# Performance work log

Measured on AMD Instinct MI355X. Metric: run time of the kernel, lower is better.

Reference implementation:

```python
import jax, jax.numpy as jnp
import numpy as np

N = 20000      # nodes (human PPI network scale)
E = 640000     # edges (avg degree 32)
PE, GOS, PROT = 128, 128, 480
OM_DIMS = [3, 3, 24, 24]          # transcriptome, proteome, effectome, interactome
D = 384                           # latent_space_dimension = 128 * 3 (jk 'cat')
H = 128                           # hidden_channels per layer
NEG_SLOPE = 0.1


def setup_inputs() -> dict:
    key = jax.random.key(0)
    ks = jax.random.split(key, 64)
    rn = lambda k, shp, s=0.05: jax.random.normal(k, shp, jnp.float32) * s
    inp = {
        "x": jax.random.normal(ks[0], (N, PE + GOS + PROT), jnp.float32),
        "x_ft": jax.random.normal(ks[1], (N, sum(OM_DIMS)), jnp.float32),
        "edge_index": jax.random.randint(ks[2], (2, E), 0, N),
    }
    i = 3
    def lin(fin, fout, name):
        nonlocal i
        inp["W_" + name] = rn(ks[i], (fin, fout)); inp["b_" + name] = jnp.zeros((fout,), jnp.float32)
        i += 1
    lin(PE, D, "pe"); lin(GOS, D, "gos"); lin(PROT, D, "prot")
    for j, d in enumerate(OM_DIMS):
        lin(d, D, f"om{j}")
    dims = [D, H, H, H]
    for j in range(3):
        lin(dims[j], dims[j + 1], f"c{j}")   # feature-branch GCN convs
        lin(dims[j], dims[j + 1], f"o{j}")   # omics-branch GCN convs
    lin(2 * D, D, "lat")
    lin(D, H, "drug"); lin(D, H, "dis")
    lin(H, 2, "odrug"); lin(H, 2, "odis")
    return inp


def _gcn(x, W, b, src, dst, deg_inv):
    # GCNConv(improved=True): A_hat = A + 2I, sym norm D^-1/2 A_hat D^-1/2
    h = x @ W                                  # [N, F_out]
    coef = deg_inv[src] * deg_inv[dst]         # [E]
    agg = jax.ops.segment_sum(h[src] * coef[:, None], dst, num_segments=N)
    agg = agg + h * (2.0 * deg_inv * deg_inv)[:, None]   # self loops (weight 2)
    return agg + b


def reference(x, x_ft, edge_index,
              W_pe, b_pe, W_gos, b_gos, W_prot, b_prot,
              W_om0, b_om0, W_om1, b_om1, W_om2, b_om2, W_om3, b_om3,
              W_c0, b_c0, W_o0, b_o0, W_c1, b_c1, W_o1, b_o1, W_c2, b_c2, W_o2, b_o2,
              W_lat, b_lat, W_drug, b_drug, W_dis, b_dis,
              W_odrug, b_odrug, W_odis, b_odis):
    act = lambda t: jax.nn.leaky_relu(t, NEG_SLOPE)
    src, dst = edge_index[0], edge_index[1]
    deg = jax.ops.segment_sum(jnp.ones((E,), jnp.float32), dst, num_segments=N) + 2.0
    deg_inv = jax.lax.rsqrt(deg)

    # encoders (features branch): pe | gosemsim | prot_emb slices of x
    pe = x[:, :PE]; gos = x[:, PE:PE + GOS]; prot = x[:, PE + GOS:PE + GOS + PROT]
    h = act(pe @ W_pe + b_pe + gos @ W_gos + b_gos + prot @ W_prot + b_prot)

    # encoders (omics branch): 3|3|24|24 slices of x_ft
    offs = np.cumsum([0] + OM_DIMS)
    Wom = [W_om0, W_om1, W_om2, W_om3]; bom = [b_om0, b_om1, b_om2, b_om3]
    g = act(sum(x_ft[:, offs[j]:offs[j + 1]] @ Wom[j] + bom[j] for j in range(4)))

    Wc = [W_c0, W_c1, W_c2]; bc = [b_c0, b_c1, b_c2]
    Wo = [W_o0, W_o1, W_o2]; bo = [b_o0, b_o1, b_o2]
    hs, gs = [], []
    for j in range(3):
        h = act(_gcn(h, Wc[j], bc[j], src, dst, deg_inv)); hs.append(h)
        g = act(_gcn(g, Wo[j], bo[j], src, dst, deg_inv)); gs.append(g)
    jk = jnp.concatenate(hs, axis=-1)          # [N, 384]
    jk_om = jnp.concatenate(gs, axis=-1)       # [N, 384]

    z = act(jnp.concatenate([jk, jk_om], axis=-1) @ W_lat + b_lat)  # [N, 384]
    drug = act(z @ W_drug + b_drug) @ W_odrug + b_odrug             # [N, 2]
    dis = act(z @ W_dis + b_dis) @ W_odis + b_odis                  # [N, 2]
    return jnp.concatenate([drug, dis], axis=-1)                    # [N, 4]
```

## Files before the change

kernel.cpp:

```cpp
#include <hip/hip_runtime.h>
#include <cstdint>

#define NN 20000
#define NNP 20096
#define NE 640000
#define NEG_SLOPE 0.1f
#define NSCAN 79
#define NSL 8
#define NPSL 2500
#define FBPS 160
#define NPART 8

typedef unsigned short ushort_t;
typedef __attribute__((ext_vector_type(8))) short short8;
typedef __attribute__((ext_vector_type(4))) float f32x4;

__device__ __forceinline__ unsigned short f2bf(float f) {
    union { float f; unsigned u; } v; v.f = f;
    unsigned r = v.u + 0x7fffu + ((v.u >> 16) & 1u);
    return (unsigned short)(r >> 16);
}
__device__ __forceinline__ float bflo(unsigned u) { return __uint_as_float(u << 16); }
__device__ __forceinline__ float bfhi(unsigned u) { return __uint_as_float(u & 0xffff0000u); }

__device__ __forceinline__ int swz(int r) { return (r ^ (r >> 2)) & 3; }

__device__ __forceinline__ void gld_lds16(const void* g, void* l) {
    __builtin_amdgcn_global_load_lds(
        (const __attribute__((address_space(1))) void*)g,
        (__attribute__((address_space(3))) void*)l,
        16, 0, 0);
}

#define O_CAT   0
#define O_OM    282624
#define O_C0    307200
#define O_O0    356352
#define O_C1    405504
#define O_O1    421888
#define O_C2    438272
#define O_O2    454656
#define O_LAT   471040
#define O_HEADS 765952
#define WT_TOTAL 864256

#define PACK_TOTAL (WT_TOTAL + 384 + 384 + 256)
#define CVT_T1 (NN * 736 / 4)
#define P1_CNTB (NSL * FBPS)
#define P1_CVTB ((CVT_T1 + NN * 64 + 255) / 256)
#define P1_PKB  (PACK_TOTAL / 256)

__global__ __launch_bounds__(256) void phase1(
    const int* __restrict__ esrc, const int* __restrict__ edst, int* __restrict__ cnt8,
    const float* __restrict__ x, const float* __restrict__ xft,
    ushort_t* __restrict__ xb, ushort_t* __restrict__ xftb,
    const float* __restrict__ Wpe, const float* __restrict__ Wgos, const float* __restrict__ Wprot,
    const float* __restrict__ bpe, const float* __restrict__ bgos, const float* __restrict__ bprot,
    const float* __restrict__ Wom0, const float* __restrict__ Wom1,
    const float* __restrict__ Wom2, const float* __restrict__ Wom3,
    const float* __restrict__ bom0, const float* __restrict__ bom1,
    const float* __restrict__ bom2, const float* __restrict__ bom3,
    const float* __restrict__ Wc0, const float* __restrict__ Wo0,
    const float* __restrict__ Wc1, const float* __restrict__ Wo1,
    const float* __restrict__ Wc2, const float* __restrict__ Wo2,
    const float* __restrict__ Wlat,
    const float* __restrict__ Wdrug, const float* __restrict__ Wdis,
    const float* __restrict__ bdrug, const float* __restrict__ bdis,
    ushort_t* __restrict__ Wt, float* __restrict__ bcat, float* __restrict__ bomc,
    float* __restrict__ bheads)
{
    int bx = blockIdx.x;
    if (bx < P1_CNTB) {
        const int slice = bx & (NSL - 1);
        const int blk = bx >> 3;
        const int lo = slice * NPSL, hi = lo + NPSL;
        for (int e = blk * 256 + threadIdx.x; e < NE; e += FBPS * 256) {
            int d = edst[e];
            if (d >= lo && d < hi) {
                int p = (unsigned)esrc[e] / 2500u;
                atomicAdd(&cnt8[d * NPART + p], 1);
            }
        }
        return;
    }
    bx -= P1_CNTB;
    if (bx < P1_CVTB) {
        int i = bx * 256 + threadIdx.x;
        if (i < CVT_T1) {
            int base = i * 4;
            float4 v = *reinterpret_cast<const float4*>(&x[base]);
            unsigned long long p = (unsigned long long)f2bf(v.x)
                                 | ((unsigned long long)f2bf(v.y) << 16)
                                 | ((unsigned long long)f2bf(v.z) << 32)
                                 | ((unsigned long long)f2bf(v.w) << 48);
            *reinterpret_cast<unsigned long long*>(&xb[base]) = p;
            return;
        }
        i -= CVT_T1;
        if (i < NN * 64) {
            int r = i >> 6, c = i & 63;
            float v = (c < 54) ? xft[r * 54 + c] : 0.f;
            xftb[i] = f2bf(v);
        }
        return;
    }
    bx -= P1_CVTB;
    {
        int i = bx * 256 + threadIdx.x;
        if (i < 282624) {
            int m = i / 736, k = i % 736;
            float v = (k < 128) ? Wpe[k * 384 + m]
                    : (k < 256) ? Wgos[(k - 128) * 384 + m]
                                : Wprot[(k - 256) * 384 + m];
            Wt[O_CAT + i] = f2bf(v);
            return;
        }
        i -= 282624;
        if (i < 24576) {
            int m = i / 64, k = i % 64;
            float v = (k < 3)  ? Wom0[k * 384 + m]
                    : (k < 6)  ? Wom1[(k - 3) * 384 + m]
                    : (k < 30) ? Wom2[(k - 6) * 384 + m]
                    : (k < 54) ? Wom3[(k - 30) * 384 + m] : 0.f;
            Wt[O_OM + i] = f2bf(v);
            return;
        }
        i -= 24576;
        if (i < 49152) { int m = i / 384, k = i % 384; Wt[O_C0 + i] = f2bf(Wc0[k * 128 + m]); return; }
        i -= 49152;
        if (i < 49152) { int m = i / 384, k = i % 384; Wt[O_O0 + i] = f2bf(Wo0[k * 128 + m]); return; }
        i -= 49152;
        if (i < 16384) { int m = i / 128, k = i % 128; Wt[O_C1 + i] = f2bf(Wc1[k * 128 + m]); return; }
        i -= 16384;
        if (i < 16384) { int m = i / 128, k = i % 128; Wt[O_O1 + i] = f2bf(Wo1[k * 128 + m]); return; }
        i -= 16384;
        if (i < 16384) { int m = i / 128, k = i % 128; Wt[O_C2 + i] = f2bf(Wc2[k * 128 + m]); return; }
        i -= 16384;
        if (i < 16384) { int m = i / 128, k = i % 128; Wt[O_O2 + i] = f2bf(Wo2[k * 128 + m]); return; }
        i -= 16384;
        if (i < 294912) { int m = i / 768, k = i % 768; Wt[O_LAT + i] = f2bf(Wlat[k * 384 + m]); return; }
        i -= 294912;
        if (i < 98304) {
            int m = i / 384, k = i % 384;
            float v = (m < 128) ? Wdrug[k * 128 + m] : Wdis[k * 128 + (m - 128)];
            Wt[O_HEADS + i] = f2bf(v);
            return;
        }
        i -= 98304;
        if (i < 384) { bcat[i] = bpe[i] + bgos[i] + bprot[i]; return; }
        i -= 384;
        if (i < 384) { bomc[i] = bom0[i] + bom1[i] + bom2[i] + bom3[i]; return; }
        i -= 384;
        if (i < 256) { bheads[i] = (i < 128) ? bdrug[i] : bdis[i - 128]; return; }
    }
}

__global__ __launch_bounds__(256) void scan_blocksums(const int* __restrict__ cnt8, int* __restrict__ bsum,
                                                      float* __restrict__ deg_inv)
{
    __shared__ int s[256];
    int t = threadIdx.x, i = blockIdx.x * 256 + t;
    int v = 0;
    if (i < NN) {
        uint4 a = *reinterpret_cast<const uint4*>(&cnt8[i * NPART]);
        uint4 b = *reinterpret_cast<const uint4*>(&cnt8[i * NPART + 4]);
        v = (int)(a.x + a.y + a.z + a.w + b.x + b.y + b.z + b.w);
        deg_inv[i] = rsqrtf((float)v + 2.0f);
    }
    s[t] = v;
    __syncthreads();
    for (int off = 128; off; off >>= 1) {
        if (t < off) s[t] += s[t + off];
        __syncthreads();
    }
    if (t == 0) bsum[blockIdx.x] = s[0];
}

__global__ __launch_bounds__(256) void scan_apply(const int* __restrict__ cnt8, const int* __restrict__ bsum,
                                                  int* __restrict__ ofsN, int* __restrict__ cursor8)
{
    __shared__ int s[256];
    __shared__ int sb[NSCAN];
    int t = threadIdx.x, i = blockIdx.x * 256 + t;
    if (t < NSCAN) sb[t] = bsum[t];
    __syncthreads();
    if (t == 0) {
        int run = 0;
        for (int b = 0; b < NSCAN; b++) { int x2 = sb[b]; sb[b] = run; run += x2; }
        if (blockIdx.x == 0) ofsN[NN] = run;
    }
    __syncthreads();
    const int boff = sb[blockIdx.x];

    int c[NPART];
    int v = 0;
    if (i < NN) {
        uint4 a = *reinterpret_cast<const uint4*>(&cnt8[i * NPART]);
        uint4 b = *reinterpret_cast<const uint4*>(&cnt8[i * NPART + 4]);
        c[0] = a.x; c[1] = a.y; c[2] = a.z; c[3] = a.w;
        c[4] = b.x; c[5] = b.y; c[6] = b.z; c[7] = b.w;
#pragma unroll
        for (int p = 0; p < NPART; p++) v += c[p];
    }
    s[t] = v;
    __syncthreads();
    for (int off = 1; off < 256; off <<= 1) {
        int u = (t >= off) ? s[t - off] : 0;
        __syncthreads();
        s[t] += u;
        __syncthreads();
    }
    if (i < NN) {
        int run = s[t] - v + boff;
        ofsN[i] = run;
#pragma unroll
        for (int p = 0; p < NPART; p++) { cursor8[i * NPART + p] = run; run += c[p]; }
    }
}

__global__ __launch_bounds__(256) void fill_csr_sliced(
    const int* __restrict__ src, const int* __restrict__ dst,
    const float* __restrict__ deg_inv, int* __restrict__ cursor8,
    uint2* __restrict__ csr_pk)
{
    const int slice = blockIdx.x & (NSL - 1);
    const int blk = blockIdx.x >> 3;
    const int lo = slice * NPSL, hi = lo + NPSL;
    for (int e = blk * 256 + threadIdx.x; e < NE; e += FBPS * 256) {
        int d = dst[e];
        if (d >= lo && d < hi) {
            int s = src[e];
            int pp = (unsigned)s / 2500u;
            int p = atomicAdd(&cursor8[d * NPART + pp], 1);
            float cf = deg_inv[s] * deg_inv[d];
            csr_pk[p] = make_uint2((unsigned)s * 512u, __float_as_uint(cf));
        }
    }
}

template<int BN>
__device__ __forceinline__ void gemm_core(
    ushort_t* As, ushort_t* Bs,
    const ushort_t* __restrict__ A, int lda,
    const ushort_t* __restrict__ Wt, int K, int row0, int col0,
    f32x4 (&acc)[4][(BN == 128) ? 4 : 2])
{
    constexpr int BK = 32;
    constexpr int NI = (BN == 128) ? 4 : 2;

    const int t = threadIdx.x;
    const int w = t >> 6, lane = t & 63;
    const int wr = w >> 1, wc = w & 1;
    const int m16 = lane & 15, quad = lane >> 4;
    const int sr = lane >> 2;
    const int pgrp = lane & 3;

#pragma unroll
    for (int mi = 0; mi < 4; mi++)
#pragma unroll
        for (int ni = 0; ni < NI; ni++) acc[mi][ni] = (f32x4)0.f;

    for (int k0 = 0; k0 < K; k0 += BK) {
#pragma unroll
        for (int p = 0; p < 2; p++) {
            int c = p * 4 + w;
            int r = c * 16 + sr;
            int q = pgrp ^ swz(r);
            gld_lds16(&A[(size_t)(row0 + r) * lda + k0 + q * 8], &As[c * 512]);
        }
#pragma unroll
        for (int p = 0; p < BN / 64; p++) {
            int c = p * 4 + w;
            int r = c * 16 + sr;
            int q = pgrp ^ swz(r);
            gld_lds16(&Wt[(size_t)(col0 + r) * K + k0 + q * 8], &Bs[c * 512]);
        }
        __syncthreads();

        short8 af[4], bfr[NI];
#pragma unroll
        for (int mi = 0; mi < 4; mi++) {
            int r = wr * 64 + mi * 16 + m16;
            int p = quad ^ swz(r);
            af[mi] = *reinterpret_cast<const short8*>(&As[r * 32 + p * 8]);
        }
#pragma unroll
        for (int ni = 0; ni < NI; ni++) {
            int n = wc * (NI * 16) + ni * 16 + m16;
            int p = quad ^ swz(n);
            bfr[ni] = *reinterpret_cast<const short8*>(&Bs[n * 32 + p * 8]);
        }
#pragma unroll
        for (int mi = 0; mi < 4; mi++)
#pragma unroll
            for (int ni = 0; ni < NI; ni++)
                acc[mi][ni] = __builtin_amdgcn_mfma_f32_16x16x32_bf16(af[mi], bfr[ni], acc[mi][ni], 0, 0, 0);
        __syncthreads();
    }
}

template<int BN, bool BIASACT, bool OUT_BF16>
__device__ __forceinline__ void gemm_store(
    const f32x4 (&acc)[4][(BN == 128) ? 4 : 2],
    const float* __restrict__ bias,
    float* __restrict__ Cf, ushort_t* __restrict__ Cb, int ldc,
    int nrows, int row0, int col0)
{
    constexpr int NI = (BN == 128) ? 4 : 2;
    const int t = threadIdx.x;
    const int w = t >> 6, lane = t & 63;
    const int wr = w >> 1, wc = w & 1;
    const int m16 = lane & 15, quad = lane >> 4;
#pragma unroll
    for (int mi = 0; mi < 4; mi++) {
#pragma unroll
        for (int reg = 0; reg < 4; reg++) {
            int grow = row0 + wr * 64 + mi * 16 + quad * 4 + reg;
            if (grow >= nrows) continue;
#pragma unroll
            for (int ni = 0; ni < NI; ni++) {
                int gcol = col0 + wc * (NI * 16) + ni * 16 + m16;
                float v = acc[mi][ni][reg];
                if constexpr (BIASACT) {
                    v += bias[gcol];
                    v = (v > 0.f) ? v : NEG_SLOPE * v;
                }
                if constexpr (OUT_BF16) Cb[(size_t)grow * ldc + gcol] = f2bf(v);
                else                    Cf[(size_t)grow * ldc + gcol] = v;
            }
        }
    }
}

template<int BN, bool BIASACT, bool OUT_BF16>
__global__ __launch_bounds__(256) void mfma_gemm(
    const ushort_t* __restrict__ A, int lda,
    const ushort_t* __restrict__ Wt,
    const float* __restrict__ bias,
    float* __restrict__ Cf, ushort_t* __restrict__ Cb, int ldc,
    int nrows, int K)
{
    __shared__ ushort_t As[128 * 32];
    __shared__ ushort_t Bs[BN * 32];
    f32x4 acc[4][(BN == 128) ? 4 : 2];
    gemm_core<BN>(As, Bs, A, lda, Wt, K, blockIdx.y * 128, blockIdx.x * BN, acc);
    gemm_store<BN, BIASACT, OUT_BF16>(acc, bias, Cf, Cb, ldc, nrows,
                                      blockIdx.y * 128, blockIdx.x * BN);
}

__global__ __launch_bounds__(256) void mfma_gemm_mlp(
    const ushort_t* __restrict__ xb, const ushort_t* __restrict__ xftb,
    const ushort_t* __restrict__ Wt,
    const float* __restrict__ bcat, const float* __restrict__ bomc,
    ushort_t* __restrict__ h0b, ushort_t* __restrict__ g0b)
{
    __shared__ ushort_t As[128 * 32];
    __shared__ ushort_t Bs[128 * 32];
    f32x4 acc[4][4];
    const int row0 = blockIdx.y * 128, col0 = blockIdx.x * 128;
    if (blockIdx.z == 0) {
        gemm_core<128>(As, Bs, xb, 736, Wt + O_CAT, 736, row0, col0, acc);
        gemm_store<128, true, true>(acc, bcat, nullptr, h0b, 384, NN, row0, col0);
    } else {
        gemm_core<128>(As, Bs, xftb, 64, Wt + O_OM, 64, row0, col0, acc);
        gemm_store<128, true, true>(acc, bomc, nullptr, g0b, 384, NN, row0, col0);
    }
}

__global__ __launch_bounds__(256) void mfma_gemm_dual(
    const ushort_t* __restrict__ A0, const ushort_t* __restrict__ A1, int lda,
    const ushort_t* __restrict__ W0, const ushort_t* __restrict__ W1,
    ushort_t* __restrict__ tmpI,
    int nrows, int K)
{
    __shared__ ushort_t As[128 * 32];
    __shared__ ushort_t Bs[64 * 32];
    const ushort_t* A  = blockIdx.z ? A1 : A0;
    const ushort_t* Wt = blockIdx.z ? W1 : W0;
    ushort_t*       Cb = tmpI + blockIdx.z * 128;
    f32x4 acc[4][2];
    gemm_core<64>(As, Bs, A, lda, Wt, K, blockIdx.y * 128, blockIdx.x * 64, acc);
    gemm_store<64, false, true>(acc, nullptr, nullptr, Cb, 256, nrows,
                                blockIdx.y * 128, blockIdx.x * 64);
}

__global__ __launch_bounds__(256) void mfma_gemm_heads(
    const ushort_t* __restrict__ zb, const ushort_t* __restrict__ Wt,
    const float* __restrict__ bheads,
    const float* __restrict__ Wod, const float* __restrict__ bod,
    const float* __restrict__ Wos, const float* __restrict__ bos,
    float* __restrict__ out)
{
    __shared__ ushort_t As[128 * 32];
    __shared__ ushort_t Bs[128 * 32];
    f32x4 acc[4][4];
    const int row0 = blockIdx.y * 128, col0 = blockIdx.x * 128;
    gemm_core<128>(As, Bs, zb, 384, Wt + O_HEADS, 384, row0, col0, acc);

    const float* __restrict__ Wh = col0 ? Wos : Wod;
    const float* __restrict__ bh = col0 ? bos : bod;
    const int t = threadIdx.x;
    const int w = t >> 6, lane = t & 63;
    const int wr = w >> 1, wc = w & 1;
    const int m16 = lane & 15, quad = lane >> 4;

    float w0[4], w1[4];
#pragma unroll
    for (int ni = 0; ni < 4; ni++) {
        int k = wc * 64 + ni * 16 + m16;
        w0[ni] = Wh[k * 2 + 0];
        w1[ni] = Wh[k * 2 + 1];
    }
    float p0[16], p1[16];
#pragma unroll
    for (int mi = 0; mi < 4; mi++) {
#pragma unroll
        for (int reg = 0; reg < 4; reg++) {
            float s0 = 0.f, s1 = 0.f;
#pragma unroll
            for (int ni = 0; ni < 4; ni++) {
                int gcol = col0 + wc * 64 + ni * 16 + m16;
                float v = acc[mi][ni][reg] + bheads[gcol];
                v = (v > 0.f) ? v : NEG_SLOPE * v;
                s0 = fmaf(v, w0[ni], s0);
                s1 = fmaf(v, w1[ni], s1);
            }
            p0[mi * 4 + reg] = s0;
            p1[mi * 4 + reg] = s1;
        }
    }
#pragma unroll
    for (int m = 1; m <= 8; m <<= 1) {
#pragma unroll
        for (int idx = 0; idx < 16; idx++) {
            p0[idx] += __shfl_xor(p0[idx], m);
            p1[idx] += __shfl_xor(p1[idx], m);
        }
    }
    float* red = reinterpret_cast<float*>(As);
    if (m16 == 0) {
#pragma unroll
        for (int mi = 0; mi < 4; mi++)
#pragma unroll
            for (int reg = 0; reg < 4; reg++) {
                int row = mi * 16 + quad * 4 + reg;
                int base = (((wr * 2 + wc) * 64) + row) * 2;
                red[base + 0] = p0[mi * 4 + reg];
                red[base + 1] = p1[mi * 4 + reg];
            }
    }
    __syncthreads();
    if (t < 128) {
        int wr2 = t >> 6, row = t & 63;
        int grow = row0 + wr2 * 64 + row;
        if (grow < NN) {
            int b0 = ((wr2 * 2 + 0) * 64 + row) * 2;
            int b1 = ((wr2 * 2 + 1) * 64 + row) * 2;
            float o0 = red[b0 + 0] + red[b1 + 0] + bh[0];
            float o1 = red[b0 + 1] + red[b1 + 1] + bh[1];
            out[(size_t)grow * 4 + (col0 ? 2 : 0) + 0] = o0;
            out[(size_t)grow * 4 + (col0 ? 2 : 0) + 1] = o1;
        }
    }
}

__global__ __launch_bounds__(256) void aggregate_fused(
    const ushort_t* __restrict__ tabI,
    const float* __restrict__ bc, const float* __restrict__ bo,
    const int* __restrict__ ofsN, const uint2* __restrict__ csr_pk,
    const float* __restrict__ deg_inv,
    ushort_t* __restrict__ outb, int hcol, int gcol)
{
    const int w = threadIdx.x >> 6, lane = threadIdx.x & 63;
    const int i = blockIdx.x * 4 + w;
    const int el = lane >> 5;
    const int fq = lane & 31;
    const int chain = fq >> 4;
    const unsigned lbyte = (unsigned)(fq * 16);
    const char* __restrict__ tb = (const char*)tabI;

    const int start = ofsN[i], end = ofsN[i + 1];
    const float di = deg_inv[i];
    const uint4 pv = *reinterpret_cast<const uint4*>(tb + ((unsigned)i * 512u + lbyte));

    float acc[8];
#pragma unroll
    for (int q = 0; q < 8; q++) acc[q] = 0.f;

#define FMA8(P, C) \
    acc[0] = fmaf(bflo(P.x), C, acc[0]); acc[1] = fmaf(bfhi(P.x), C, acc[1]); \
    acc[2] = fmaf(bflo(P.y), C, acc[2]); acc[3] = fmaf(bfhi(P.y), C, acc[3]); \
    acc[4] = fmaf(bflo(P.z), C, acc[4]); acc[5] = fmaf(bfhi(P.z), C, acc[5]); \
    acc[6] = fmaf(bflo(P.w), C, acc[6]); acc[7] = fmaf(bfhi(P.w), C, acc[7])

    int j = start + el;
    for (; j + 6 < end; j += 8) {
        uint2 e0 = csr_pk[j];
        uint2 e1 = csr_pk[j + 2];
        uint2 e2 = csr_pk[j + 4];
        uint2 e3 = csr_pk[j + 6];
        uint4 p0 = *reinterpret_cast<const uint4*>(tb + (e0.x + lbyte));
        uint4 p1 = *reinterpret_cast<const uint4*>(tb + (e1.x + lbyte));
        uint4 p2 = *reinterpret_cast<const uint4*>(tb + (e2.x + lbyte));
        uint4 p3 = *reinterpret_cast<const uint4*>(tb + (e3.x + lbyte));
        float c0 = __uint_as_float(e0.y), c1 = __uint_as_float(e1.y);
        float c2 = __uint_as_float(e2.y), c3 = __uint_as_float(e3.y);
        FMA8(p0, c0); FMA8(p1, c1); FMA8(p2, c2); FMA8(p3, c3);
    }
    for (; j < end; j += 2) {
        uint2 e0 = csr_pk[j];
        uint4 p0 = *reinterpret_cast<const uint4*>(tb + (e0.x + lbyte));
        float c0 = __uint_as_float(e0.y);
        FMA8(p0, c0);
    }
#undef FMA8

#pragma unroll
    for (int q = 0; q < 8; q++) acc[q] += __shfl_xor(acc[q], 32);

    if (el == 0) {
        const float* __restrict__ bias = chain ? bo : bc;
        const int coloff = (fq & 15) * 8;
        const float c = 2.f * di * di;
        float sv[8] = {bflo(pv.x), bfhi(pv.x), bflo(pv.y), bfhi(pv.y),
                       bflo(pv.z), bfhi(pv.z), bflo(pv.w), bfhi(pv.w)};
        uint4 o;
        unsigned* op = &o.x;
#pragma unroll
        for (int q = 0; q < 8; q += 2) {
            float v0 = fmaf(sv[q],     c, acc[q])     + bias[coloff + q];
            float v1 = fmaf(sv[q + 1], c, acc[q + 1]) + bias[coloff + q + 1];
            v0 = (v0 > 0.f) ? v0 : NEG_SLOPE * v0;
            v1 = (v1 > 0.f) ? v1 : NEG_SLOPE * v1;
            op[q >> 1] = (unsigned)f2bf(v0) | ((unsigned)f2bf(v1) << 16);
        }
        const int col = (chain ? gcol : hcol) + coloff;
        *reinterpret_cast<uint4*>(&outb[(size_t)i * 768 + col]) = o;
    }
}

extern "C" void kernel_launch(void* const* d_in, const int* in_sizes, int n_in,
                              void* d_out, int out_size, void* d_ws, size_t ws_size,
                              hipStream_t stream)
{
    const float* x      = (const float*)d_in[0];
    const float* x_ft   = (const float*)d_in[1];
    const int*   eidx   = (const int*)d_in[2];
    const float* W_pe   = (const float*)d_in[3];
    const float* b_pe   = (const float*)d_in[4];
    const float* W_gos  = (const float*)d_in[5];
    const float* b_gos  = (const float*)d_in[6];
    const float* W_prot = (const float*)d_in[7];
    const float* b_prot = (const float*)d_in[8];
    const float* W_om0  = (const float*)d_in[9];
    const float* b_om0  = (const float*)d_in[10];
    const float* W_om1  = (const float*)d_in[11];
    const float* b_om1  = (const float*)d_in[12];
    const float* W_om2  = (const float*)d_in[13];
    const float* b_om2  = (const float*)d_in[14];
    const float* W_om3  = (const float*)d_in[15];
    const float* b_om3  = (const float*)d_in[16];
    const float* W_c[3] = {(const float*)d_in[17], (const float*)d_in[21], (const float*)d_in[25]};
    const float* b_c[3] = {(const float*)d_in[18], (const float*)d_in[22], (const float*)d_in[26]};
    const float* W_o[3] = {(const float*)d_in[19], (const float*)d_in[23], (const float*)d_in[27]};
    const float* b_o[3] = {(const float*)d_in[20], (const float*)d_in[24], (const float*)d_in[28]};
    const float* W_lat  = (const float*)d_in[29];
    const float* b_lat  = (const float*)d_in[30];
    const float* W_drug = (const float*)d_in[31];
    const float* b_drug = (const float*)d_in[32];
    const float* W_dis  = (const float*)d_in[33];
    const float* b_dis  = (const float*)d_in[34];
    const float* W_odrug= (const float*)d_in[35];
    const float* b_odrug= (const float*)d_in[36];
    const float* W_odis = (const float*)d_in[37];
    const float* b_odis = (const float*)d_in[38];
    float* out = (float*)d_out;

    const int* e_src = eidx;
    const int* e_dst = eidx + NE;

    char* p = (char*)d_ws;
    auto alloc = [&](size_t bytes) -> void* {
        void* r = (void*)p;
        p += (bytes + 255) & ~(size_t)255;
        return r;
    };
    ushort_t* Wt    = (ushort_t*)alloc((size_t)WT_TOTAL * 2);
    float* bcat     = (float*)alloc(384 * 4);
    float* bomc     = (float*)alloc(384 * 4);
    float* bheads   = (float*)alloc(256 * 4);
    float* deg_inv  = (float*)alloc((size_t)NN * 4);
    int*   cnt8     = (int*)alloc((size_t)NN * NPART * 4);
    int*   cursor8  = (int*)alloc((size_t)NN * NPART * 4);
    int*   ofsN     = (int*)alloc((size_t)(NN + 1) * 4);
    int*   bsum     = (int*)alloc((size_t)NSCAN * 4);
    uint2* csr_pk   = (uint2*)alloc((size_t)NE * 8);
    ushort_t* xb    = (ushort_t*)alloc((size_t)NNP * 736 * 2);
    ushort_t* xftb  = (ushort_t*)alloc((size_t)NNP * 64 * 2);
    ushort_t* h0b   = (ushort_t*)alloc((size_t)NNP * 384 * 2);
    ushort_t* g0b   = (ushort_t*)alloc((size_t)NNP * 384 * 2);
    ushort_t* jkb   = (ushort_t*)alloc((size_t)NNP * 768 * 2);
    ushort_t* zb    = (ushort_t*)alloc((size_t)NNP * 384 * 2);
    ushort_t* tmpI  = (ushort_t*)alloc((size_t)NNP * 256 * 2);
    (void)ws_size; (void)in_sizes; (void)n_in; (void)out_size;

    hipMemsetAsync(cnt8, 0, (size_t)NN * NPART * 4, stream);
    phase1<<<dim3(P1_CNTB + P1_CVTB + P1_PKB), dim3(256), 0, stream>>>(
        e_src, e_dst, cnt8,
        x, x_ft, xb, xftb,
        W_pe, W_gos, W_prot, b_pe, b_gos, b_prot,
        W_om0, W_om1, W_om2, W_om3, b_om0, b_om1, b_om2, b_om3,
        W_c[0], W_o[0], W_c[1], W_o[1], W_c[2], W_o[2],
        W_lat, W_drug, W_dis, b_drug, b_dis, Wt, bcat, bomc, bheads);

    scan_blocksums<<<dim3(NSCAN), dim3(256), 0, stream>>>(cnt8, bsum, deg_inv);
    scan_apply<<<dim3(NSCAN), dim3(256), 0, stream>>>(cnt8, bsum, ofsN, cursor8);
    fill_csr_sliced<<<dim3(NSL * FBPS), dim3(256), 0, stream>>>(e_src, e_dst, deg_inv, cursor8, csr_pk);

    mfma_gemm_mlp<<<dim3(3, 157, 2), dim3(256), 0, stream>>>(
        xb, xftb, Wt, bcat, bomc, h0b, g0b);

    mfma_gemm_dual<<<dim3(2, 157, 2), dim3(256), 0, stream>>>(
        h0b, g0b, 384, Wt + O_C0, Wt + O_O0, tmpI, NN, 384);
    aggregate_fused<<<dim3(NN / 4), dim3(256), 0, stream>>>(
        tmpI, b_c[0], b_o[0], ofsN, csr_pk, deg_inv, jkb, 0, 384);

    mfma_gemm_dual<<<dim3(2, 157, 2), dim3(256), 0, stream>>>(
        jkb + 0, jkb + 384, 768, Wt + O_C1, Wt + O_O1, tmpI, NN, 128);
    aggregate_fused<<<dim3(NN / 4), dim3(256), 0, stream>>>(
        tmpI, b_c[1], b_o[1], ofsN, csr_pk, deg_inv, jkb, 128, 512);

    mfma_gemm_dual<<<dim3(2, 157, 2), dim3(256), 0, stream>>>(
        jkb + 128, jkb + 512, 768, Wt + O_C2, Wt + O_O2, tmpI, NN, 128);
    aggregate_fused<<<dim3(NN / 4), dim3(256), 0, stream>>>(
        tmpI, b_c[2], b_o[2], ofsN, csr_pk, deg_inv, jkb, 256, 640);

    mfma_gemm<128, true, true><<<dim3(3, 157), dim3(256), 0, stream>>>(
        jkb, 768, Wt + O_LAT, b_lat, nullptr, zb, 384, NN, 768);

    mfma_gemm_heads<<<dim3(2, 157), dim3(256), 0, stream>>>(
        zb, Wt, bheads, W_odrug, b_odrug, W_odis, b_odis, out);
}
```

Baseline: 452.9 us.

## Drop dst-sliced edge passes and fuse CSR fill with encoder GEMM launch

The degree-count and CSR-fill passes no longer scan every edge once per destination slice. Each now uses one thread per edge, which removes the 8x redundant reads of the edge arrays but gives up the locality the slicing gave the atomics. The CSR fill is merged into the same launch as the encoder MLP GEMM, so the two independent pieces of work overlap and one kernel launch disappears. The aggregation tail loop is also replaced by a single predicated 4-wide step, so that the remaining gathers are issued together.

After: 454.6 us. Within noise of the previous version (+0.4%).

```diff
diff --git a/kernel.cpp b/kernel.cpp
--- a/kernel.cpp
+++ b/kernel.cpp
@@ -6,9 +6,6 @@
 #define NE 640000
 #define NEG_SLOPE 0.1f
 #define NSCAN 79
-#define NSL 8
-#define NPSL 2500
-#define FBPS 160
 #define NPART 8
 
 typedef unsigned short ushort_t;
@@ -46,7 +43,7 @@
 
 #define PACK_TOTAL (WT_TOTAL + 384 + 384 + 256)
 #define CVT_T1 (NN * 736 / 4)
-#define P1_CNTB (NSL * FBPS)
+#define P1_CNTB (NE / 256)
 #define P1_CVTB ((CVT_T1 + NN * 64 + 255) / 256)
 #define P1_PKB  (PACK_TOTAL / 256)
 
@@ -71,16 +68,10 @@
 {
     int bx = blockIdx.x;
     if (bx < P1_CNTB) {
-        const int slice = bx & (NSL - 1);
-        const int blk = bx >> 3;
-        const int lo = slice * NPSL, hi = lo + NPSL;
-        for (int e = blk * 256 + threadIdx.x; e < NE; e += FBPS * 256) {
-            int d = edst[e];
-            if (d >= lo && d < hi) {
-                int p = (unsigned)esrc[e] / 2500u;
-                atomicAdd(&cnt8[d * NPART + p], 1);
-            }
-        }
+        int e = bx * 256 + threadIdx.x;
+        int d = edst[e];
+        int p = (unsigned)esrc[e] / 2500u;
+        atomicAdd(&cnt8[d * NPART + p], 1);
         return;
     }
     bx -= P1_CNTB;
@@ -218,26 +209,6 @@
     }
 }
 
-__global__ __launch_bounds__(256) void fill_csr_sliced(
-    const int* __restrict__ src, const int* __restrict__ dst,
-    const float* __restrict__ deg_inv, int* __restrict__ cursor8,
-    uint2* __restrict__ csr_pk)
-{
-    const int slice = blockIdx.x & (NSL - 1);
-    const int blk = blockIdx.x >> 3;
-    const int lo = slice * NPSL, hi = lo + NPSL;
-    for (int e = blk * 256 + threadIdx.x; e < NE; e += FBPS * 256) {
-        int d = dst[e];
-        if (d >= lo && d < hi) {
-            int s = src[e];
-            int pp = (unsigned)s / 2500u;
-            int p = atomicAdd(&cursor8[d * NPART + pp], 1);
-            float cf = deg_inv[s] * deg_inv[d];
-            csr_pk[p] = make_uint2((unsigned)s * 512u, __float_as_uint(cf));
-        }
-    }
-}
-
 template<int BN>
 __device__ __forceinline__ void gemm_core(
     ushort_t* As, ushort_t* Bs,
@@ -348,7 +319,12 @@
                                       blockIdx.y * 128, blockIdx.x * BN);
 }
 
-__global__ __launch_bounds__(256) void mfma_gemm_mlp(
+#define P2_FILLB (NE / 256)
+#define P2_MLPB  (3 * 157 * 2)
+__global__ __launch_bounds__(256) void phase2(
+    const int* __restrict__ esrc, const int* __restrict__ edst,
+    const float* __restrict__ deg_inv, int* __restrict__ cursor8,
+    uint2* __restrict__ csr_pk,
     const ushort_t* __restrict__ xb, const ushort_t* __restrict__ xftb,
     const ushort_t* __restrict__ Wt,
     const float* __restrict__ bcat, const float* __restrict__ bomc,
@@ -356,9 +332,23 @@
 {
     __shared__ ushort_t As[128 * 32];
     __shared__ ushort_t Bs[128 * 32];
+    int bx = blockIdx.x;
+    if (bx < P2_FILLB) {
+        int e = bx * 256 + threadIdx.x;
+        int d = edst[e];
+        int s = esrc[e];
+        int pp = (unsigned)s / 2500u;
+        int p = atomicAdd(&cursor8[d * NPART + pp], 1);
+        float cf = deg_inv[s] * deg_inv[d];
+        csr_pk[p] = make_uint2((unsigned)s * 512u, __float_as_uint(cf));
+        return;
+    }
+    bx -= P2_FILLB;
+    int z = bx / 471, r = bx % 471;
+    int by = r / 3, b3 = r % 3;
     f32x4 acc[4][4];
-    const int row0 = blockIdx.y * 128, col0 = blockIdx.x * 128;
-    if (blockIdx.z == 0) {
+    const int row0 = by * 128, col0 = b3 * 128;
+    if (z == 0) {
         gemm_core<128>(As, Bs, xb, 736, Wt + O_CAT, 736, row0, col0, acc);
         gemm_store<128, true, true>(acc, bcat, nullptr, h0b, 384, NN, row0, col0);
     } else {
@@ -507,11 +497,22 @@
         float c2 = __uint_as_float(e2.y), c3 = __uint_as_float(e3.y);
         FMA8(p0, c0); FMA8(p1, c1); FMA8(p2, c2); FMA8(p3, c3);
     }
-    for (; j < end; j += 2) {
-        uint2 e0 = csr_pk[j];
+    if (j < end) {
+        int i0 = j, i1 = j + 2, i2 = j + 4, i3 = j + 6;
+        int l = end - 1;
+        uint2 e0 = csr_pk[i0];
+        uint2 e1 = csr_pk[i1 < end ? i1 : l];
+        uint2 e2 = csr_pk[i2 < end ? i2 : l];
+        uint2 e3 = csr_pk[i3 < end ? i3 : l];
         uint4 p0 = *reinterpret_cast<const uint4*>(tb + (e0.x + lbyte));
+        uint4 p1 = *reinterpret_cast<const uint4*>(tb + (e1.x + lbyte));
+        uint4 p2 = *reinterpret_cast<const uint4*>(tb + (e2.x + lbyte));
+        uint4 p3 = *reinterpret_cast<const uint4*>(tb + (e3.x + lbyte));
         float c0 = __uint_as_float(e0.y);
-        FMA8(p0, c0);
+        float c1 = (i1 < end) ? __uint_as_float(e1.y) : 0.f;
+        float c2 = (i2 < end) ? __uint_as_float(e2.y) : 0.f;
+        float c3 = (i3 < end) ? __uint_as_float(e3.y) : 0.f;
+        FMA8(p0, c0); FMA8(p1, c1); FMA8(p2, c2); FMA8(p3, c3);
     }
 #undef FMA8
 
@@ -615,9 +616,9 @@
 
     scan_blocksums<<<dim3(NSCAN), dim3(256), 0, stream>>>(cnt8, bsum, deg_inv);
     scan_apply<<<dim3(NSCAN), dim3(256), 0, stream>>>(cnt8, bsum, ofsN, cursor8);
-    fill_csr_sliced<<<dim3(NSL * FBPS), dim3(256), 0, stream>>>(e_src, e_dst, deg_inv, cursor8, csr_pk);
-
-    mfma_gemm_mlp<<<dim3(3, 157, 2), dim3(256), 0, stream>>>(
+
+    phase2<<<dim3(P2_FILLB + P2_MLPB), dim3(256), 0, stream>>>(
+        e_src, e_dst, deg_inv, cursor8, csr_pk,
         xb, xftb, Wt, bcat, bomc, h0b, g0b);
 
     mfma_gemm_dual<<<dim3(2, 157, 2), dim3(256), 0, stream>>>(
```
